# Optimization experiments

Measured on AMD Instinct MI355X. Metric: run time of the kernel, lower is better.

The kernel has to match this reference:

```python
import jax, jax.numpy as jnp
import numpy as np

B, NP, NJ, ND = 16, 64, 15, 128
SIGMA = 15.0        # cfg.MULTI_PERSON.POSE_SIGMA
BIG = 1.0e5         # sentinel used to mask padded reference persons
EPS = 1e-8


def setup_inputs() -> dict:
    key = jax.random.key(0)
    k1, k2, k3, k4, k5 = jax.random.split(key, 5)
    # 3D plane-sweep hypotheses in the reference camera frame (z>0 so projection is safe)
    uv = jax.random.uniform(k1, (B, NP, NJ, ND, 2), minval=-0.5, maxval=0.5)
    z = jax.random.uniform(k2, (B, NP, NJ, ND, 1), minval=2.0, maxval=10.0)
    poses_3d = jnp.concatenate([uv * z, z], axis=-1).astype(jnp.float32)
    # detected 2D poses in the reference view, pixel coordinates
    poses_2d_ref = (jax.random.uniform(k3, (B, NP, NJ, 2)) * jnp.array([1920.0, 1080.0], jnp.float32)).astype(jnp.float32)
    vis_ref = (jax.random.uniform(k4, (B, NP, NJ)) < 0.8).astype(jnp.float32)
    num_persons_ref = jax.random.randint(k5, (B,), 1, NP + 1).astype(jnp.int32)
    R = jnp.tile(jnp.eye(3, dtype=jnp.float32), (B, 1, 1))
    T = jnp.zeros((B, 3), jnp.float32)
    f = jnp.full((B, 2), 1000.0, jnp.float32)
    c = jnp.tile(jnp.array([960.0, 540.0], jnp.float32), (B, 1))
    image_w = jnp.full((B,), 1920.0, jnp.float32)
    image_h = jnp.full((B,), 1080.0, jnp.float32)
    return dict(poses_3d=poses_3d, poses_2d_ref=poses_2d_ref, vis_ref=vis_ref,
                num_persons_ref=num_persons_ref, R=R, T=T, f=f, c=c,
                image_w=image_w, image_h=image_h)


def _project(pts, R, T, f, c):
    # pinhole projection: x_cam = R (X - T); 2d = f * xy/z + c
    xc = jnp.einsum('bij,bpkdj->bpkdi', R, pts - T[:, None, None, None, :])
    z = xc[..., 2:3]
    return f[:, None, None, None, :] * xc[..., :2] / z + c[:, None, None, None, :]


def reference(poses_3d, poses_2d_ref, vis_ref, num_persons_ref, R, T, f, c, image_w, image_h):
    # 1) project 3D hypotheses to the reference view -> [B,NP,NJ,ND,2]
    p2t = _project(poses_3d, R, T, f, c)
    # 2) visibility-weighted mean pairwise squared distance, expanded as
    #    |a|^2 + |b|^2 - 2 a.b to avoid the [B,NP,NP,NJ,ND,2] intermediate
    pt2 = jnp.sum(p2t ** 2, axis=-1)                      # [B,NP,NJ,ND]
    pr2 = jnp.sum(poses_2d_ref ** 2, axis=-1)             # [B,NQ,NJ]
    wpr = poses_2d_ref * vis_ref[..., None]               # [B,NQ,NJ,2]
    term1 = jnp.einsum('bpjd,bqj->bpqd', pt2, vis_ref)
    term2 = jnp.sum(pr2 * vis_ref, axis=-1)               # [B,NQ]
    term3 = jnp.einsum('bpjdc,bqjc->bpqd', p2t, wpr)
    vsum = jnp.sum(vis_ref, axis=-1)                      # [B,NQ]
    dist = (term1 + term2[:, None, :, None] - 2.0 * term3) / (vsum[:, None, :, None] + EPS)
    # 3) mask padded reference persons, nearest-pose matching
    valid = jnp.arange(NP)[None, :] < num_persons_ref[:, None]   # [B,NQ]
    dist = jnp.where(valid[:, None, :, None], dist, BIG)
    mm = jnp.argmin(dist, axis=2)                          # [B,NP,ND]
    # 4) gather matched 2D poses / visibilities
    b_idx = jnp.arange(B)[:, None, None]
    matched = jnp.transpose(poses_2d_ref[b_idx, mm], (0, 1, 3, 2, 4))  # [B,NP,NJ,ND,2]
    mvis = jnp.transpose(vis_ref[b_idx, mm], (0, 1, 3, 2))             # [B,NP,NJ,ND]
    # 5) exp score (non-panoptic branch) and in-image bounding
    mdist = jnp.sum((p2t - matched) ** 2, axis=-1)
    score = jnp.exp(-mdist / (SIGMA ** 2))
    iw = image_w[:, None, None, None]
    ih = image_h[:, None, None, None]
    inb = ((p2t[..., 0] >= 0) & (p2t[..., 1] >= 0) &
           (p2t[..., 0] <= iw - 1) & (p2t[..., 1] <= ih - 1)).astype(score.dtype)
    bounding = inb * mvis
    return score * bounding
```

## Files before the change

kernel.cpp:

```cpp
#include <hip/hip_runtime.h>

#define NPERS 64
#define NJOINT 15
#define NDEPTH 128
#define BIGF 100000.0f
#define EPSF 1e-8f
#define INFF 3.0e38f

#define F4E(v, e) ((e) == 0 ? (v).x : (e) == 1 ? (v).y : (e) == 2 ? (v).z : (v).w)

__global__ __launch_bounds__(256, 4)
void pose_match_kernel(
    const float* __restrict__ poses_3d,
    const float* __restrict__ p2d,
    const float* __restrict__ vis,
    const int*   __restrict__ nper,
    const float* __restrict__ Rm,
    const float* __restrict__ Tm,
    const float* __restrict__ fm,
    const float* __restrict__ cm,
    const float* __restrict__ iw_,
    const float* __restrict__ ih_,
    float* __restrict__ out)
{
    const int b    = blockIdx.x >> 6;
    const int rem  = blockIdx.x & 63;
    const int pp   = rem >> 1;
    const int dh   = rem & 1;
    const int p0   = pp * 2;
    const int tid  = threadIdx.x;
    const int wv   = tid >> 6;
    const int lane = tid & 63;
    const int d    = dh * 64 + lane;

    __shared__ float4 sq[NPERS][NJOINT];
    __shared__ float4 sco[NPERS][12];
    __shared__ float  bvred[4][2][64];
    __shared__ int    bqred[4][2][64];

    for (int i = tid; i < NPERS * NJOINT; i += 256) {
        int q = i / NJOINT, j = i % NJOINT;
        float v  = vis[(b * NPERS + q) * NJOINT + j];
        float rx = p2d[((b * NPERS + q) * NJOINT + j) * 2 + 0];
        float ry = p2d[((b * NPERS + q) * NJOINT + j) * 2 + 1];
        sq[q][j] = make_float4(v, rx, ry, 0.0f);
    }
    __syncthreads();

    if (tid < NPERS) {
        const int q = tid;
        float vs = 0.0f, t2 = 0.0f;
        #pragma unroll
        for (int j = 0; j < NJOINT; ++j) {
            float4 s = sq[q][j];
            vs += s.x;
            t2 = fmaf(s.y * s.y + s.z * s.z, s.x, t2);
        }
        float inv = 1.0f / (vs + EPSF);
        float* o = (float*)&sco[q][0];
        #pragma unroll
        for (int j = 0; j < NJOINT; ++j) {
            float4 s = sq[q][j];
            o[j]      = s.x * inv;
            o[16 + j] = 2.0f * s.x * s.y * inv;
            o[32 + j] = 2.0f * s.x * s.z * inv;
        }
        o[15] = t2 * inv;
        o[31] = 0.0f;
        o[47] = 0.0f;
    }
    __syncthreads();

    const float R00 = Rm[b*9+0], R01 = Rm[b*9+1], R02 = Rm[b*9+2];
    const float R10 = Rm[b*9+3], R11 = Rm[b*9+4], R12 = Rm[b*9+5];
    const float R20 = Rm[b*9+6], R21 = Rm[b*9+7], R22 = Rm[b*9+8];
    const float T0 = Tm[b*3+0], T1 = Tm[b*3+1], T2 = Tm[b*3+2];
    const float fx = fm[b*2+0], fy = fm[b*2+1];
    const float cx = cm[b*2+0], cy = cm[b*2+1];
    const float iwm1 = iw_[b] - 1.0f;
    const float ihm1 = ih_[b] - 1.0f;
    const int   npv  = nper[b];

    float X0[NJOINT], Y0[NJOINT], X1[NJOINT], Y1[NJOINT];
    #pragma unroll
    for (int j = 0; j < NJOINT; ++j) {
        int base = (((b * NPERS + p0) * NJOINT + j) * NDEPTH + d) * 3;
        float a0 = poses_3d[base + 0] - T0;
        float a1 = poses_3d[base + 1] - T1;
        float a2 = poses_3d[base + 2] - T2;
        float xc0 = R00 * a0 + R01 * a1 + R02 * a2;
        float xc1 = R10 * a0 + R11 * a1 + R12 * a2;
        float xc2 = R20 * a0 + R21 * a1 + R22 * a2;
        float r   = __builtin_amdgcn_rcpf(xc2);
        X0[j] = fmaf(fx * xc0, r, cx);
        Y0[j] = fmaf(fy * xc1, r, cy);
    }
    #pragma unroll
    for (int j = 0; j < NJOINT; ++j) {
        int base = (((b * NPERS + p0 + 1) * NJOINT + j) * NDEPTH + d) * 3;
        float a0 = poses_3d[base + 0] - T0;
        float a1 = poses_3d[base + 1] - T1;
        float a2 = poses_3d[base + 2] - T2;
        float xc0 = R00 * a0 + R01 * a1 + R02 * a2;
        float xc1 = R10 * a0 + R11 * a1 + R12 * a2;
        float xc2 = R20 * a0 + R21 * a1 + R22 * a2;
        float r   = __builtin_amdgcn_rcpf(xc2);
        X1[j] = fmaf(fx * xc0, r, cx);
        Y1[j] = fmaf(fy * xc1, r, cy);
    }

    float bv0, bv1;
    int   bq0, bq1;
    if (npv < NPERS) { bv0 = bv1 = BIGF; bq0 = bq1 = npv; }
    else             { bv0 = bv1 = INFF; bq0 = bq1 = 0;   }

    for (int q = wv; q < npv; q += 4) {
        const float c = sco[q][3].w;
        float a0 = c, a1 = c;
        #pragma unroll
        for (int k = 0; k < 4; ++k) {
            float4 cw4 = sco[q][k];
            float4 cx4 = sco[q][4 + k];
            float4 cy4 = sco[q][8 + k];
            #pragma unroll
            for (int e = 0; e < 4; ++e) {
                if (k == 3 && e == 3) continue;
                const int j = k * 4 + e;
                float w  = F4E(cw4, e);
                float wx = F4E(cx4, e);
                float wy = F4E(cy4, e);
                float u;
                u = fmaf(w, X0[j], -wx); a0 = fmaf(X0[j], u, a0);
                u = fmaf(w, Y0[j], -wy); a0 = fmaf(Y0[j], u, a0);
                u = fmaf(w, X1[j], -wx); a1 = fmaf(X1[j], u, a1);
                u = fmaf(w, Y1[j], -wy); a1 = fmaf(Y1[j], u, a1);
            }
        }
        if (a0 < bv0) { bv0 = a0; bq0 = q; }
        if (a1 < bv1) { bv1 = a1; bq1 = q; }
    }
    bvred[wv][0][lane] = bv0;  bqred[wv][0][lane] = bq0;
    bvred[wv][1][lane] = bv1;  bqred[wv][1][lane] = bq1;
    __syncthreads();

#define EPILOGUE(PI, XA, YA)                                                  \
    if (wv == PI) {                                                           \
        float bestv = bvred[0][PI][lane];                                     \
        int   bestq = bqred[0][PI][lane];                                     \
        _Pragma("unroll")                                                     \
        for (int k = 1; k < 4; ++k) {                                         \
            float v  = bvred[k][PI][lane];                                    \
            int   qq = bqred[k][PI][lane];                                    \
            if (v < bestv || (v == bestv && qq < bestq)) {                    \
                bestv = v; bestq = qq;                                        \
            }                                                                 \
        }                                                                     \
        const int obase = ((b * NPERS + p0 + PI) * NJOINT) * NDEPTH + d;      \
        _Pragma("unroll")                                                     \
        for (int j = 0; j < NJOINT; ++j) {                                    \
            float4 v = sq[bestq][j];                                          \
            float xx = XA[j], yy = YA[j];                                     \
            float dx = xx - v.y;                                              \
            float dy = yy - v.z;                                              \
            float md = fmaf(dx, dx, dy * dy);                                 \
            float sc = __expf(-md * (1.0f / 225.0f));                         \
            float inb = (xx >= 0.0f && yy >= 0.0f &&                          \
                         xx <= iwm1 && yy <= ihm1) ? 1.0f : 0.0f;             \
            out[obase + j * NDEPTH] = sc * inb * v.x;                         \
        }                                                                     \
    }

    EPILOGUE(0, X0, Y0)
    EPILOGUE(1, X1, Y1)
#undef EPILOGUE
}

extern "C" void kernel_launch(void* const* d_in, const int* in_sizes, int n_in,
                              void* d_out, int out_size, void* d_ws, size_t ws_size,
                              hipStream_t stream) {
    const float* poses_3d = (const float*)d_in[0];
    const float* p2d      = (const float*)d_in[1];
    const float* vis      = (const float*)d_in[2];
    const int*   nper     = (const int*)d_in[3];
    const float* Rm       = (const float*)d_in[4];
    const float* Tm       = (const float*)d_in[5];
    const float* fm       = (const float*)d_in[6];
    const float* cm       = (const float*)d_in[7];
    const float* iw       = (const float*)d_in[8];
    const float* ih       = (const float*)d_in[9];
    float* out = (float*)d_out;

    const int B = in_sizes[3];
    dim3 grid(B * 64);
    dim3 block(256);
    pose_match_kernel<<<grid, block, 0, stream>>>(
        poses_3d, p2d, vis, nper, Rm, Tm, fm, cm, iw, ih, out);
}
```

Measured before the change: 29.16 us.

## Swap loop order: stream joints outer, accumulate 16 persons per wave in registers

The distance loop is restructured so each wave owns a fixed block of 16 reference persons and iterates over joints in the outer loop. Projected coordinates are computed per joint and discarded, so the per-thread X/Y arrays go away. The coefficient table is transposed to a joint-major shared layout, and the epilogue re-reads and re-projects the 3D poses instead of keeping them in registers. The goal is lower register pressure and fewer shared loads per FMA, at the cost of redundant global loads and projection in the epilogue and per-wave work imbalance when few persons are valid.

```diff
diff --git a/kernel.cpp b/kernel.cpp
--- a/kernel.cpp
+++ b/kernel.cpp
@@ -6,8 +6,6 @@
 #define BIGF 100000.0f
 #define EPSF 1e-8f
 #define INFF 3.0e38f
-
-#define F4E(v, e) ((e) == 0 ? (v).x : (e) == 1 ? (v).y : (e) == 2 ? (v).z : (v).w)
 
 __global__ __launch_bounds__(256, 4)
 void pose_match_kernel(
@@ -34,7 +32,8 @@
     const int d    = dh * 64 + lane;
 
     __shared__ float4 sq[NPERS][NJOINT];
-    __shared__ float4 sco[NPERS][12];
+    __shared__ float4 sco2[NJOINT][48];
+    __shared__ float  sc_c[NPERS];
     __shared__ float  bvred[4][2][64];
     __shared__ int    bqred[4][2][64];
 
@@ -57,17 +56,15 @@
             t2 = fmaf(s.y * s.y + s.z * s.z, s.x, t2);
         }
         float inv = 1.0f / (vs + EPSF);
-        float* o = (float*)&sco[q][0];
         #pragma unroll
         for (int j = 0; j < NJOINT; ++j) {
             float4 s = sq[q][j];
-            o[j]      = s.x * inv;
-            o[16 + j] = 2.0f * s.x * s.y * inv;
-            o[32 + j] = 2.0f * s.x * s.z * inv;
-        }
-        o[15] = t2 * inv;
-        o[31] = 0.0f;
-        o[47] = 0.0f;
+            float* row = (float*)&sco2[j][0];
+            row[q * 3 + 0] = s.x * inv;
+            row[q * 3 + 1] = 2.0f * s.x * s.y * inv;
+            row[q * 3 + 2] = 2.0f * s.x * s.z * inv;
+        }
+        sc_c[q] = t2 * inv;
     }
     __syncthreads();
 
@@ -81,69 +78,89 @@
     const float ihm1 = ih_[b] - 1.0f;
     const int   npv  = nper[b];
 
-    float X0[NJOINT], Y0[NJOINT], X1[NJOINT], Y1[NJOINT];
+    const int q0 = wv * 16;
+    const int nv = min(max(npv - q0, 0), 16);
+
+    const float* pA = poses_3d + ((size_t)(b * NPERS + p0    ) * NJOINT * NDEPTH + d) * 3;
+    const float* pB = poses_3d + ((size_t)(b * NPERS + p0 + 1) * NJOINT * NDEPTH + d) * 3;
+
+    float acc[2][16];
     #pragma unroll
+    for (int k = 0; k < 16; ++k) { acc[0][k] = 0.0f; acc[1][k] = 0.0f; }
+
+    #pragma unroll 1
     for (int j = 0; j < NJOINT; ++j) {
-        int base = (((b * NPERS + p0) * NJOINT + j) * NDEPTH + d) * 3;
-        float a0 = poses_3d[base + 0] - T0;
-        float a1 = poses_3d[base + 1] - T1;
-        float a2 = poses_3d[base + 2] - T2;
-        float xc0 = R00 * a0 + R01 * a1 + R02 * a2;
-        float xc1 = R10 * a0 + R11 * a1 + R12 * a2;
-        float xc2 = R20 * a0 + R21 * a1 + R22 * a2;
-        float r   = __builtin_amdgcn_rcpf(xc2);
-        X0[j] = fmaf(fx * xc0, r, cx);
-        Y0[j] = fmaf(fy * xc1, r, cy);
-    }
-    #pragma unroll
-    for (int j = 0; j < NJOINT; ++j) {
-        int base = (((b * NPERS + p0 + 1) * NJOINT + j) * NDEPTH + d) * 3;
-        float a0 = poses_3d[base + 0] - T0;
-        float a1 = poses_3d[base + 1] - T1;
-        float a2 = poses_3d[base + 2] - T2;
-        float xc0 = R00 * a0 + R01 * a1 + R02 * a2;
-        float xc1 = R10 * a0 + R11 * a1 + R12 * a2;
-        float xc2 = R20 * a0 + R21 * a1 + R22 * a2;
-        float r   = __builtin_amdgcn_rcpf(xc2);
-        X1[j] = fmaf(fx * xc0, r, cx);
-        Y1[j] = fmaf(fy * xc1, r, cy);
+        const int off = j * NDEPTH * 3;
+        float X0, Y0, X1, Y1;
+        {
+            float a0 = pA[off + 0] - T0;
+            float a1 = pA[off + 1] - T1;
+            float a2 = pA[off + 2] - T2;
+            float xc0 = R00 * a0 + R01 * a1 + R02 * a2;
+            float xc1 = R10 * a0 + R11 * a1 + R12 * a2;
+            float xc2 = R20 * a0 + R21 * a1 + R22 * a2;
+            float r   = __builtin_amdgcn_rcpf(xc2);
+            X0 = fmaf(fx * xc0, r, cx);
+            Y0 = fmaf(fy * xc1, r, cy);
+        }
+        {
+            float a0 = pB[off + 0] - T0;
+            float a1 = pB[off + 1] - T1;
+            float a2 = pB[off + 2] - T2;
+            float xc0 = R00 * a0 + R01 * a1 + R02 * a2;
+            float xc1 = R10 * a0 + R11 * a1 + R12 * a2;
+            float xc2 = R20 * a0 + R21 * a1 + R22 * a2;
+            float r   = __builtin_amdgcn_rcpf(xc2);
+            X1 = fmaf(fx * xc0, r, cx);
+            Y1 = fmaf(fy * xc1, r, cy);
+        }
+
+        #pragma unroll
+        for (int g = 0; g < 4; ++g) {
+            if (g * 4 < nv) {
+                float4 r0 = sco2[j][wv * 12 + g * 3 + 0];
+                float4 r1 = sco2[j][wv * 12 + g * 3 + 1];
+                float4 r2 = sco2[j][wv * 12 + g * 3 + 2];
+#define ACC1(K, W, WX, WY)                                                    \
+                {                                                             \
+                    float u;                                                  \
+                    u = fmaf((W), X0, -(WX));                                 \
+                    acc[0][g * 4 + K] = fmaf(X0, u, acc[0][g * 4 + K]);       \
+                    u = fmaf((W), Y0, -(WY));                                 \
+                    acc[0][g * 4 + K] = fmaf(Y0, u, acc[0][g * 4 + K]);       \
+                    u = fmaf((W), X1, -(WX));                                 \
+                    acc[1][g * 4 + K] = fmaf(X1, u, acc[1][g * 4 + K]);       \
+                    u = fmaf((W), Y1, -(WY));                                 \
+                    acc[1][g * 4 + K] = fmaf(Y1, u, acc[1][g * 4 + K]);       \
+                }
+                ACC1(0, r0.x, r0.y, r0.z)
+                ACC1(1, r0.w, r1.x, r1.y)
+                ACC1(2, r1.z, r1.w, r2.x)
+                ACC1(3, r2.y, r2.z, r2.w)
+#undef ACC1
+            }
+        }
     }
 
     float bv0, bv1;
     int   bq0, bq1;
     if (npv < NPERS) { bv0 = bv1 = BIGF; bq0 = bq1 = npv; }
     else             { bv0 = bv1 = INFF; bq0 = bq1 = 0;   }
-
-    for (int q = wv; q < npv; q += 4) {
-        const float c = sco[q][3].w;
-        float a0 = c, a1 = c;
-        #pragma unroll
-        for (int k = 0; k < 4; ++k) {
-            float4 cw4 = sco[q][k];
-            float4 cx4 = sco[q][4 + k];
-            float4 cy4 = sco[q][8 + k];
-            #pragma unroll
-            for (int e = 0; e < 4; ++e) {
-                if (k == 3 && e == 3) continue;
-                const int j = k * 4 + e;
-                float w  = F4E(cw4, e);
-                float wx = F4E(cx4, e);
-                float wy = F4E(cy4, e);
-                float u;
-                u = fmaf(w, X0[j], -wx); a0 = fmaf(X0[j], u, a0);
-                u = fmaf(w, Y0[j], -wy); a0 = fmaf(Y0[j], u, a0);
-                u = fmaf(w, X1[j], -wx); a1 = fmaf(X1[j], u, a1);
-                u = fmaf(w, Y1[j], -wy); a1 = fmaf(Y1[j], u, a1);
-            }
-        }
-        if (a0 < bv0) { bv0 = a0; bq0 = q; }
-        if (a1 < bv1) { bv1 = a1; bq1 = q; }
+    #pragma unroll
+    for (int k = 0; k < 16; ++k) {
+        if (k < nv) {
+            float cterm = sc_c[q0 + k];
+            float d0 = acc[0][k] + cterm;
+            float d1 = acc[1][k] + cterm;
+            if (d0 < bv0) { bv0 = d0; bq0 = q0 + k; }
+            if (d1 < bv1) { bv1 = d1; bq1 = q0 + k; }
+        }
     }
     bvred[wv][0][lane] = bv0;  bqred[wv][0][lane] = bq0;
     bvred[wv][1][lane] = bv1;  bqred[wv][1][lane] = bq1;
     __syncthreads();
 
-#define EPILOGUE(PI, XA, YA)                                                  \
+#define EPILOGUE(PI, PPTR)                                                    \
     if (wv == PI) {                                                           \
         float bestv = bvred[0][PI][lane];                                     \
         int   bestq = bqred[0][PI][lane];                                     \
@@ -158,8 +175,17 @@
         const int obase = ((b * NPERS + p0 + PI) * NJOINT) * NDEPTH + d;      \
         _Pragma("unroll")                                                     \
         for (int j = 0; j < NJOINT; ++j) {                                    \
+            const int off = j * NDEPTH * 3;                                   \
+            float a0 = PPTR[off + 0] - T0;                                    \
+            float a1 = PPTR[off + 1] - T1;                                    \
+            float a2 = PPTR[off + 2] - T2;                                    \
+            float xc0 = R00 * a0 + R01 * a1 + R02 * a2;                       \
+            float xc1 = R10 * a0 + R11 * a1 + R12 * a2;                       \
+            float xc2 = R20 * a0 + R21 * a1 + R22 * a2;                       \
+            float r   = __builtin_amdgcn_rcpf(xc2);                           \
+            float xx  = fmaf(fx * xc0, r, cx);                                \
+            float yy  = fmaf(fy * xc1, r, cy);                                \
             float4 v = sq[bestq][j];                                          \
-            float xx = XA[j], yy = YA[j];                                     \
             float dx = xx - v.y;                                              \
             float dy = yy - v.z;                                              \
             float md = fmaf(dx, dx, dy * dy);                                 \
@@ -170,8 +196,8 @@
         }                                                                     \
     }
 
-    EPILOGUE(0, X0, Y0)
-    EPILOGUE(1, X1, Y1)
+    EPILOGUE(0, pA)
+    EPILOGUE(1, pB)
 #undef EPILOGUE
 }
 
```

New measurement: 42.20 us. +44.7%, slower.
